# Performance work log

Measured on AMD Instinct MI355X. Metric: run time of the kernel, lower is better.

## Reference

```python
import jax, jax.numpy as jnp
import numpy as np

B = 2048
WIDTH = 128      # channel width == 1D signal length after unsqueeze
MODES = 16       # retained Fourier modes
INPUT_DIM = 100
T_DIM = 28
U_DIM = 64
NFREQ = WIDTH // 2 + 1


def setup_inputs() -> dict:
    key = jax.random.key(0)
    ks = jax.random.split(key, 32)
    rn = lambda k, s: jax.random.normal(k, s, jnp.float32)
    un = lambda k, s: jax.random.uniform(k, s, jnp.float32)
    sc_in0 = 1.0 / (1 * WIDTH)        # SpectralConv scale for conv0 (in=1)
    sc_in = 1.0 / (WIDTH * WIDTH)     # for conv1..3
    inp = {
        "X1": rn(ks[0], (B, INPUT_DIM + T_DIM)),
        "fc0_w": rn(ks[1], (WIDTH, INPUT_DIM + T_DIM)) * 0.02,
        "fc0_b": jnp.zeros((WIDTH,), jnp.float32),
        # spectral weights: torch.rand(..., cfloat) -> uniform real & imag in [0,1), scaled
        "sc0_wr": un(ks[2], (1, WIDTH, MODES)) * sc_in0,
        "sc0_wi": un(ks[3], (1, WIDTH, MODES)) * sc_in0,
        "sc1_wr": un(ks[4], (WIDTH, WIDTH, MODES)) * sc_in,
        "sc1_wi": un(ks[5], (WIDTH, WIDTH, MODES)) * sc_in,
        "sc2_wr": un(ks[6], (WIDTH, WIDTH, MODES)) * sc_in,
        "sc2_wi": un(ks[7], (WIDTH, WIDTH, MODES)) * sc_in,
        "sc3_wr": un(ks[8], (WIDTH, WIDTH, MODES)) * sc_in,
        "sc3_wi": un(ks[9], (WIDTH, WIDTH, MODES)) * sc_in,
        # pointwise (kernel-size-1) Conv1d weights as [out, in] + bias
        "w0_w": rn(ks[10], (WIDTH, 1)) * 0.02,
        "w0_b": jnp.zeros((WIDTH,), jnp.float32),
        "w1_w": rn(ks[11], (WIDTH, WIDTH)) * 0.02,
        "w1_b": jnp.zeros((WIDTH,), jnp.float32),
        "w2_w": rn(ks[12], (WIDTH, WIDTH)) * 0.02,
        "w2_b": jnp.zeros((WIDTH,), jnp.float32),
        "w3_w": rn(ks[13], (WIDTH, WIDTH)) * 0.02,
        "w3_b": jnp.zeros((WIDTH,), jnp.float32),
        "fc1_w": rn(ks[14], (WIDTH, WIDTH * WIDTH)) * 0.01,
        "fc1_b": jnp.zeros((WIDTH,), jnp.float32),
        "fc2_w": rn(ks[15], (U_DIM, WIDTH)) * 0.02,
        "fc2_b": jnp.zeros((U_DIM,), jnp.float32),
    }
    return inp


def _spectral_conv(x, wr, wi):
    # x: [B, Cin, L]; wr/wi: [Cin, Cout, MODES]
    L = x.shape[-1]
    xf = jnp.fft.rfft(x)                                   # [B, Cin, L//2+1] complex
    w = wr + 1j * wi
    of = jnp.einsum('bim,iom->bom', xf[:, :, :MODES], w)   # [B, Cout, MODES]
    of = jnp.pad(of, ((0, 0), (0, 0), (0, L // 2 + 1 - MODES)))
    return jnp.fft.irfft(of, n=L)                          # [B, Cout, L] real


def _pointwise(x, w, b):
    # kernel-size-1 Conv1d: x [B, Cin, L], w [Cout, Cin], b [Cout]
    return jnp.einsum('bil,oi->bol', x, w) + b[None, :, None]


def _gelu(x):
    return jax.nn.gelu(x, approximate=False)  # torch F.gelu default (erf)


def reference(X1, fc0_w, fc0_b, sc0_wr, sc0_wi, sc1_wr, sc1_wi, sc2_wr, sc2_wi,
              sc3_wr, sc3_wi, w0_w, w0_b, w1_w, w1_b, w2_w, w2_b, w3_w, w3_b,
              fc1_w, fc1_b, fc2_w, fc2_b):
    # fc0: lift [B, input_dim+t_dim] -> [B, width]
    x = X1 @ fc0_w.T + fc0_b
    x = x[:, None, :]  # [B, 1, WIDTH]
    x = _gelu(_spectral_conv(x, sc0_wr, sc0_wi) + _pointwise(x, w0_w, w0_b))
    x = _gelu(_spectral_conv(x, sc1_wr, sc1_wi) + _pointwise(x, w1_w, w1_b))
    x = _gelu(_spectral_conv(x, sc2_wr, sc2_wi) + _pointwise(x, w2_w, w2_b))
    x = _spectral_conv(x, sc3_wr, sc3_wi) + _pointwise(x, w3_w, w3_b)
    x = x.reshape(x.shape[0], -1)              # [B, WIDTH*WIDTH]
    x = _gelu(x @ fc1_w.T + fc1_b)
    x = x @ fc2_w.T + fc2_b                    # [B, U_DIM]
    return jnp.squeeze(x)
```

## Files before the change

### kernel.cpp

```cpp
#include <hip/hip_runtime.h>
#include <math.h>

#define PI_D 3.14159265358979323846

#define OFF_TW   0u
#define OFF_X0   4096u
#define OFF_WT   (OFF_X0 + 262144u)
#define OFF_XFR  (OFF_WT + 1572864u)
#define OFF_XFI  (OFF_XFR + 4194304u)
#define OFF_OFR  (OFF_XFI + 4194304u)
#define OFF_OFI  (OFF_OFR + 4194304u)
#define OFF_A    (OFF_OFI + 4194304u)
#define OFF_HP   OFF_XFR

__device__ __forceinline__ float gelu_f(float x) {
    return 0.5f * x * (1.0f + erff(x * 0.7071067811865476f));
}

__global__ void k_setup(float* ws) {
    int id = blockIdx.x * 256 + threadIdx.x;
    if (id < 4096) {
        int l = id >> 5, c = id & 31, m = c & 15;
        double ang = (PI_D / 64.0) * (double)((m * l) & 127);
        double v = (c < 16) ? cos(ang) : -sin(ang);
        ws[OFF_TW + id] = (float)v;
    }
}

__global__ void k_transpose(const float* w1r, const float* w1i,
                            const float* w2r, const float* w2i,
                            const float* w3r, const float* w3i, float* ws) {
    int id = blockIdx.x * 256 + threadIdx.x;
    int lay = id >> 18;
    int rem = id & 262143;
    int m = rem >> 14, i = (rem >> 7) & 127, o = rem & 127;
    const float* sr = (lay == 0) ? w1r : (lay == 1) ? w2r : w3r;
    const float* si = (lay == 0) ? w1i : (lay == 1) ? w2i : w3i;
    int src = (i * 128 + o) * 16 + m;
    ws[OFF_WT + (unsigned)lay * 524288u + rem] = sr[src];
    ws[OFF_WT + (unsigned)lay * 524288u + 262144u + rem] = si[src];
}

__global__ __launch_bounds__(256) void k_fc0(const float* X1, const float* w, const float* bias, float* ws) {
    __shared__ float xs[16][128];
    __shared__ float wsm[128][129];
    int t = threadIdx.x;
    int b0 = blockIdx.x * 16;
#pragma unroll
    for (int q = 0; q < 8; ++q) {
        int idx = q * 256 + t;
        xs[idx >> 7][idx & 127] = X1[b0 * 128 + idx];
    }
#pragma unroll
    for (int q = 0; q < 64; ++q) {
        int idx = q * 256 + t;
        wsm[idx >> 7][idx & 127] = w[idx];
    }
    __syncthreads();
    int c = t & 127, bh = t >> 7;
    float* x0 = ws + OFF_X0;
    for (int j = 0; j < 8; ++j) {
        int b = bh * 8 + j;
        float acc = bias[c];
#pragma unroll 8
        for (int k = 0; k < 128; ++k) acc += xs[b][k] * wsm[c][k];
        x0[(b0 + b) * 128 + c] = acc;
    }
}

__global__ __launch_bounds__(256) void k_layer0(const float* w0r, const float* w0i,
                                                const float* w0w, const float* w0b, float* ws) {
    __shared__ float x0s[128];
    __shared__ float tws[128][33];
    __shared__ float xrs[16], xis[16];
    __shared__ __align__(16) float ors[2048];
    __shared__ __align__(16) float ois[2048];
    int t = threadIdx.x, b = blockIdx.x;
    const float* tw = ws + OFF_TW;
    const float* x0 = ws + OFF_X0;
    if (t < 128) x0s[t] = x0[b * 128 + t];
#pragma unroll
    for (int q = 0; q < 16; ++q) {
        int idx = q * 256 + t;
        tws[idx >> 5][idx & 31] = tw[idx];
    }
    __syncthreads();
    if (t < 32) {
        float acc = 0.f;
        for (int l = 0; l < 128; ++l) acc += x0s[l] * tws[l][t];
        if (t < 16) xrs[t] = acc; else xis[t - 16] = acc;
    }
    __syncthreads();
#pragma unroll
    for (int q = 0; q < 8; ++q) {
        int idx = q * 256 + t;
        int m = idx & 15;
        float wr = w0r[idx], wi = w0i[idx];
        float sc = (m == 0) ? (1.f / 128.f) : (2.f / 128.f);
        float xr = xrs[m], xi = xis[m];
        ors[idx] = (xr * wr - xi * wi) * sc;
        ois[idx] = (xr * wi + xi * wr) * sc;
    }
    __syncthreads();
    int l = t & 127, og = t >> 7;
    float tvc[16], tvs[16];
#pragma unroll
    for (int m = 0; m < 16; ++m) { tvc[m] = tws[l][m]; tvs[m] = tws[l][16 + m]; }
    float xl = x0s[l];
    float* A = ws + OFF_A + b * 16384;
    const float4* or4 = (const float4*)ors;
    const float4* oi4 = (const float4*)ois;
    for (int oj = 0; oj < 64; ++oj) {
        int o = og * 64 + oj;
        float acc = xl * w0w[o] + w0b[o];
#pragma unroll
        for (int q = 0; q < 4; ++q) {
            float4 r4 = or4[o * 4 + q];
            float4 i4 = oi4[o * 4 + q];
            acc += r4.x * tvc[4 * q + 0] + i4.x * tvs[4 * q + 0];
            acc += r4.y * tvc[4 * q + 1] + i4.y * tvs[4 * q + 1];
            acc += r4.z * tvc[4 * q + 2] + i4.z * tvs[4 * q + 2];
            acc += r4.w * tvc[4 * q + 3] + i4.w * tvs[4 * q + 3];
        }
        A[o * 128 + l] = gelu_f(acc);
    }
}

__global__ __launch_bounds__(256) void k_dft(float* ws) {
    __shared__ float as_[16][516];
    __shared__ float tws_[16][32];
    int t = threadIdx.x;
    int row0 = blockIdx.x * 512;
    const float* A = ws + OFF_A;
    const float* tw = ws + OFF_TW;
    int tr = t >> 2, tc = t & 3;
    float acc[8][8];
#pragma unroll
    for (int j = 0; j < 8; ++j)
#pragma unroll
        for (int cc = 0; cc < 8; ++cc) acc[j][cc] = 0.f;
    for (int kc = 0; kc < 8; ++kc) {
        int k0 = kc * 16;
        __syncthreads();
#pragma unroll
        for (int q = 0; q < 8; ++q) {
            int idx = q * 256 + t;
            int r = idx >> 2, kq = idx & 3;
            float4 v = *(const float4*)&A[(row0 + r) * 128 + k0 + 4 * kq];
            as_[4 * kq + 0][r] = v.x; as_[4 * kq + 1][r] = v.y;
            as_[4 * kq + 2][r] = v.z; as_[4 * kq + 3][r] = v.w;
        }
#pragma unroll
        for (int q = 0; q < 2; ++q) {
            int idx = q * 256 + t;
            tws_[idx >> 5][idx & 31] = tw[(k0 + (idx >> 5)) * 32 + (idx & 31)];
        }
        __syncthreads();
#pragma unroll 8
        for (int kk = 0; kk < 16; ++kk) {
            float4 a0 = *(const float4*)&as_[kk][tr * 8];
            float4 a1 = *(const float4*)&as_[kk][tr * 8 + 4];
            float4 t0 = *(const float4*)&tws_[kk][tc * 8];
            float4 t1 = *(const float4*)&tws_[kk][tc * 8 + 4];
            float av[8] = {a0.x,a0.y,a0.z,a0.w,a1.x,a1.y,a1.z,a1.w};
            float tv[8] = {t0.x,t0.y,t0.z,t0.w,t1.x,t1.y,t1.z,t1.w};
#pragma unroll
            for (int j = 0; j < 8; ++j)
#pragma unroll
                for (int cc = 0; cc < 8; ++cc) acc[j][cc] += av[j] * tv[cc];
        }
    }
    float* xfr = ws + OFF_XFR;
    float* xfi = ws + OFF_XFI;
#pragma unroll
    for (int cc = 0; cc < 8; ++cc) {
        int c = tc * 8 + cc;
        float* dst = (c < 16) ? (xfr + c * 262144) : (xfi + (c - 16) * 262144);
        float4 v0 = make_float4(acc[0][cc], acc[1][cc], acc[2][cc], acc[3][cc]);
        float4 v1 = make_float4(acc[4][cc], acc[5][cc], acc[6][cc], acc[7][cc]);
        *(float4*)&dst[row0 + tr * 8] = v0;
        *(float4*)&dst[row0 + tr * 8 + 4] = v1;
    }
}

__global__ __launch_bounds__(256) void k_modemix(int lay, float* ws) {
    __shared__ float xrs[32][68], xis[32][68];
    __shared__ float wrs[32][128], wis[32][128];
    int t = threadIdx.x;
    int b0 = blockIdx.x * 64;
    int m = blockIdx.y;
    const float* xfr = ws + OFF_XFR + m * 262144;
    const float* xfi = ws + OFF_XFI + m * 262144;
    const float* wtr = ws + OFF_WT + (unsigned)lay * 524288u + m * 16384;
    const float* wti = wtr + 262144;
    int tb = t >> 4, tc = t & 15;
    float accr[4][8], acci[4][8];
#pragma unroll
    for (int jb = 0; jb < 4; ++jb)
#pragma unroll
        for (int jc = 0; jc < 8; ++jc) { accr[jb][jc] = 0.f; acci[jb][jc] = 0.f; }
    for (int kc = 0; kc < 4; ++kc) {
        int k0 = kc * 32;
        __syncthreads();
#pragma unroll
        for (int q = 0; q < 2; ++q) {
            int idx = q * 256 + t;
            int r = idx >> 3, kq = idx & 7;
            float4 vr = *(const float4*)&xfr[(b0 + r) * 128 + k0 + 4 * kq];
            float4 vi = *(const float4*)&xfi[(b0 + r) * 128 + k0 + 4 * kq];
            xrs[4*kq+0][r] = vr.x; xrs[4*kq+1][r] = vr.y; xrs[4*kq+2][r] = vr.z; xrs[4*kq+3][r] = vr.w;
            xis[4*kq+0][r] = vi.x; xis[4*kq+1][r] = vi.y; xis[4*kq+2][r] = vi.z; xis[4*kq+3][r] = vi.w;
        }
#pragma unroll
        for (int q = 0; q < 4; ++q) {
            int idx = q * 256 + t;
            int kk = idx >> 5, oq = idx & 31;
            *(float4*)&wrs[kk][4*oq] = *(const float4*)&wtr[(k0 + kk) * 128 + 4*oq];
            *(float4*)&wis[kk][4*oq] = *(const float4*)&wti[(k0 + kk) * 128 + 4*oq];
        }
        __syncthreads();
#pragma unroll 4
        for (int kk = 0; kk < 32; ++kk) {
            float4 xr4 = *(const float4*)&xrs[kk][tb * 4];
            float4 xi4 = *(const float4*)&xis[kk][tb * 4];
            float4 wr0 = *(const float4*)&wrs[kk][tc * 8];
            float4 wr1 = *(const float4*)&wrs[kk][tc * 8 + 4];
            float4 wi0 = *(const float4*)&wis[kk][tc * 8];
            float4 wi1 = *(const float4*)&wis[kk][tc * 8 + 4];
            float xrv[4] = {xr4.x, xr4.y, xr4.z, xr4.w};
            float xiv[4] = {xi4.x, xi4.y, xi4.z, xi4.w};
            float wrv[8] = {wr0.x,wr0.y,wr0.z,wr0.w,wr1.x,wr1.y,wr1.z,wr1.w};
            float wiv[8] = {wi0.x,wi0.y,wi0.z,wi0.w,wi1.x,wi1.y,wi1.z,wi1.w};
#pragma unroll
            for (int jb = 0; jb < 4; ++jb)
#pragma unroll
                for (int jc = 0; jc < 8; ++jc) {
                    accr[jb][jc] += xrv[jb] * wrv[jc] - xiv[jb] * wiv[jc];
                    acci[jb][jc] += xrv[jb] * wiv[jc] + xiv[jb] * wrv[jc];
                }
        }
    }
    float* ofr = ws + OFF_OFR + m * 262144;
    float* ofi = ws + OFF_OFI + m * 262144;
#pragma unroll
    for (int jb = 0; jb < 4; ++jb) {
        int b = b0 + tb * 4 + jb;
        float4 r0 = make_float4(accr[jb][0], accr[jb][1], accr[jb][2], accr[jb][3]);
        float4 r1 = make_float4(accr[jb][4], accr[jb][5], accr[jb][6], accr[jb][7]);
        float4 i0 = make_float4(acci[jb][0], acci[jb][1], acci[jb][2], acci[jb][3]);
        float4 i1 = make_float4(acci[jb][4], acci[jb][5], acci[jb][6], acci[jb][7]);
        *(float4*)&ofr[b * 128 + tc * 8]     = r0;
        *(float4*)&ofr[b * 128 + tc * 8 + 4] = r1;
        *(float4*)&ofi[b * 128 + tc * 8]     = i0;
        *(float4*)&ofi[b * 128 + tc * 8 + 4] = i1;
    }
}

template <int GELU>
__global__ __launch_bounds__(256) void k_layerB(const float* pw_w, const float* pw_b, float* ws) {
    __shared__ float ofr_s[16][128], ofi_s[16][128];
    __shared__ float as_[32][128];
    __shared__ float wsx[32][132];
    int t = threadIdx.x, b = blockIdx.x;
    const float* tw = ws + OFF_TW;
    float* A = ws + OFF_A + b * 16384;
    const float* ofr = ws + OFF_OFR;
    const float* ofi = ws + OFF_OFI;
    int ty = t >> 4, tx = t & 15;
    float bv[8];
#pragma unroll
    for (int jo = 0; jo < 8; ++jo) bv[jo] = pw_b[ty * 8 + jo];
#pragma unroll
    for (int q = 0; q < 2; ++q) {
        int idx = q * 256 + t;
        int mm = idx >> 5, oq = idx & 31;
        float sc = (mm == 0) ? (1.f / 128.f) : (2.f / 128.f);
        float4 vr = *(const float4*)&ofr[mm * 262144 + b * 128 + 4 * oq];
        float4 vi = *(const float4*)&ofi[mm * 262144 + b * 128 + 4 * oq];
        vr.x *= sc; vr.y *= sc; vr.z *= sc; vr.w *= sc;
        vi.x *= sc; vi.y *= sc; vi.z *= sc; vi.w *= sc;
        *(float4*)&ofr_s[mm][4 * oq] = vr;
        *(float4*)&ofi_s[mm][4 * oq] = vi;
    }
    float acc[8][8];
#pragma unroll
    for (int jo = 0; jo < 8; ++jo)
#pragma unroll
        for (int jl = 0; jl < 8; ++jl) acc[jo][jl] = 0.f;
    for (int ch = 0; ch < 4; ++ch) {
        int i0 = ch * 32;
        __syncthreads();
#pragma unroll
        for (int q = 0; q < 4; ++q) {
            int idx = q * 256 + t;
            int ic = idx >> 5, lq = idx & 31;
            *(float4*)&as_[ic][4 * lq] = *(const float4*)&A[(i0 + ic) * 128 + 4 * lq];
        }
#pragma unroll
        for (int q = 0; q < 4; ++q) {
            int idx = q * 256 + t;
            int o = idx >> 3, iq = idx & 7;
            float4 v = *(const float4*)&pw_w[o * 128 + i0 + 4 * iq];
            wsx[4*iq+0][o] = v.x; wsx[4*iq+1][o] = v.y; wsx[4*iq+2][o] = v.z; wsx[4*iq+3][o] = v.w;
        }
        __syncthreads();
#pragma unroll 4
        for (int ic = 0; ic < 32; ++ic) {
            float4 a0 = *(const float4*)&as_[ic][tx * 8];
            float4 a1 = *(const float4*)&as_[ic][tx * 8 + 4];
            float4 w0 = *(const float4*)&wsx[ic][ty * 8];
            float4 w1 = *(const float4*)&wsx[ic][ty * 8 + 4];
            float av[8] = {a0.x,a0.y,a0.z,a0.w,a1.x,a1.y,a1.z,a1.w};
            float wv[8] = {w0.x,w0.y,w0.z,w0.w,w1.x,w1.y,w1.z,w1.w};
#pragma unroll
            for (int jo = 0; jo < 8; ++jo)
#pragma unroll
                for (int jl = 0; jl < 8; ++jl) acc[jo][jl] += wv[jo] * av[jl];
        }
    }
    __syncthreads();
    float (*twsA)[33] = (float(*)[33])wsx;
#pragma unroll
    for (int q = 0; q < 4; ++q) {
        int idx = q * 256 + t;
        int l = idx >> 3, cq = idx & 7;
        float4 v = *(const float4*)&tw[l * 32 + 4 * cq];
        twsA[l][4*cq+0] = v.x; twsA[l][4*cq+1] = v.y; twsA[l][4*cq+2] = v.z; twsA[l][4*cq+3] = v.w;
    }
    __syncthreads();
#pragma unroll 2
    for (int m = 0; m < 16; ++m) {
        float orv[8], oiv[8];
#pragma unroll
        for (int jo = 0; jo < 8; ++jo) { orv[jo] = ofr_s[m][ty * 8 + jo]; oiv[jo] = ofi_s[m][ty * 8 + jo]; }
        float cv[8], sv[8];
#pragma unroll
        for (int jl = 0; jl < 8; ++jl) {
            int l = tx * 8 + jl;
            cv[jl] = twsA[l][m]; sv[jl] = twsA[l][16 + m];
        }
#pragma unroll
        for (int jo = 0; jo < 8; ++jo)
#pragma unroll
            for (int jl = 0; jl < 8; ++jl) acc[jo][jl] += orv[jo] * cv[jl] + oiv[jo] * sv[jl];
    }
#pragma unroll
    for (int jo = 0; jo < 8; ++jo) {
        int o = ty * 8 + jo;
        float v[8];
#pragma unroll
        for (int jl = 0; jl < 8; ++jl) {
            float x = acc[jo][jl] + bv[jo];
            v[jl] = GELU ? gelu_f(x) : x;
        }
        *(float4*)&A[o * 128 + tx * 8]     = make_float4(v[0], v[1], v[2], v[3]);
        *(float4*)&A[o * 128 + tx * 8 + 4] = make_float4(v[4], v[5], v[6], v[7]);
    }
}

__global__ __launch_bounds__(256) void k_fc12(const float* fc1w, float* ws) {
    __shared__ float as_[32][132];
    __shared__ float ws_[32][132];
    int t = threadIdx.x;
    int b0 = blockIdx.x * 128;
    int kz = blockIdx.y;
    const float* A = ws + OFF_A;
    int tm = t >> 4, tn = t & 15;
    float acc[8][8];
#pragma unroll
    for (int jb = 0; jb < 8; ++jb)
#pragma unroll
        for (int jc = 0; jc < 8; ++jc) acc[jb][jc] = 0.f;
    for (int ks = 0; ks < 8; ++ks) {
        int k0 = kz * 256 + ks * 32;
        __syncthreads();
#pragma unroll
        for (int q = 0; q < 4; ++q) {
            int idx = q * 256 + t;
            int r = idx >> 3, kq = idx & 7;
            float4 v = *(const float4*)&A[(b0 + r) * 16384 + k0 + 4 * kq];
            as_[4*kq+0][r] = v.x; as_[4*kq+1][r] = v.y; as_[4*kq+2][r] = v.z; as_[4*kq+3][r] = v.w;
        }
#pragma unroll
        for (int q = 0; q < 4; ++q) {
            int idx = q * 256 + t;
            int c = idx >> 3, kq = idx & 7;
            float4 v = *(const float4*)&fc1w[c * 16384 + k0 + 4 * kq];
            ws_[4*kq+0][c] = v.x; ws_[4*kq+1][c] = v.y; ws_[4*kq+2][c] = v.z; ws_[4*kq+3][c] = v.w;
        }
        __syncthreads();
#pragma unroll 4
        for (int kk = 0; kk < 32; ++kk) {
            float4 a0 = *(const float4*)&as_[kk][tm * 8];
            float4 a1 = *(const float4*)&as_[kk][tm * 8 + 4];
            float4 w0 = *(const float4*)&ws_[kk][tn * 8];
            float4 w1 = *(const float4*)&ws_[kk][tn * 8 + 4];
            float av[8] = {a0.x,a0.y,a0.z,a0.w,a1.x,a1.y,a1.z,a1.w};
            float wv[8] = {w0.x,w0.y,w0.z,w0.w,w1.x,w1.y,w1.z,w1.w};
#pragma unroll
            for (int jb = 0; jb < 8; ++jb)
#pragma unroll
                for (int jc = 0; jc < 8; ++jc) acc[jb][jc] += av[jb] * wv[jc];
        }
    }
    float* hp = ws + OFF_HP + kz * 262144;
#pragma unroll
    for (int jb = 0; jb < 8; ++jb) {
        int b = b0 + tm * 8 + jb;
        *(float4*)&hp[b * 128 + tn * 8]     = make_float4(acc[jb][0], acc[jb][1], acc[jb][2], acc[jb][3]);
        *(float4*)&hp[b * 128 + tn * 8 + 4] = make_float4(acc[jb][4], acc[jb][5], acc[jb][6], acc[jb][7]);
    }
}

__global__ __launch_bounds__(256) void k_fc2(const float* fc1b, const float* fc2w, const float* fc2b,
                                             float* ws, float* out) {
    __shared__ float hs[8][128];
    __shared__ float w2s[64][129];
    int t = threadIdx.x;
    int b0 = blockIdx.x * 8;
    const float* hp = ws + OFF_HP;
#pragma unroll
    for (int q = 0; q < 4; ++q) {
        int idx = q * 256 + t;
        int bb = idx >> 7, c = idx & 127;
        float s = fc1b[c];
#pragma unroll 8
        for (int kz = 0; kz < 64; ++kz) s += hp[kz * 262144 + (b0 + bb) * 128 + c];
        hs[bb][c] = gelu_f(s);
    }
#pragma unroll
    for (int q = 0; q < 32; ++q) {
        int idx = q * 256 + t;
        w2s[idx >> 7][idx & 127] = fc2w[idx];
    }
    __syncthreads();
#pragma unroll
    for (int q = 0; q < 2; ++q) {
        int idx = q * 256 + t;
        int bb = idx >> 6, u = idx & 63;
        float acc = fc2b[u];
#pragma unroll 8
        for (int c = 0; c < 128; ++c) acc += hs[bb][c] * w2s[u][c];
        out[(b0 + bb) * 64 + u] = acc;
    }
}

extern "C" void kernel_launch(void* const* d_in, const int* in_sizes, int n_in,
                              void* d_out, int out_size, void* d_ws, size_t ws_size,
                              hipStream_t stream) {
    const float* X1   = (const float*)d_in[0];
    const float* fc0w = (const float*)d_in[1];
    const float* fc0b = (const float*)d_in[2];
    const float* s0r  = (const float*)d_in[3];
    const float* s0i  = (const float*)d_in[4];
    const float* s1r  = (const float*)d_in[5];
    const float* s1i  = (const float*)d_in[6];
    const float* s2r  = (const float*)d_in[7];
    const float* s2i  = (const float*)d_in[8];
    const float* s3r  = (const float*)d_in[9];
    const float* s3i  = (const float*)d_in[10];
    const float* w0w  = (const float*)d_in[11];
    const float* w0b  = (const float*)d_in[12];
    const float* w1w  = (const float*)d_in[13];
    const float* w1b  = (const float*)d_in[14];
    const float* w2w  = (const float*)d_in[15];
    const float* w2b  = (const float*)d_in[16];
    const float* w3w  = (const float*)d_in[17];
    const float* w3b  = (const float*)d_in[18];
    const float* fc1w = (const float*)d_in[19];
    const float* fc1b = (const float*)d_in[20];
    const float* fc2w = (const float*)d_in[21];
    const float* fc2b = (const float*)d_in[22];
    float* ws  = (float*)d_ws;
    float* out = (float*)d_out;

    k_setup<<<dim3(16), dim3(256), 0, stream>>>(ws);
    k_transpose<<<dim3(3072), dim3(256), 0, stream>>>(s1r, s1i, s2r, s2i, s3r, s3i, ws);
    k_fc0<<<dim3(128), dim3(256), 0, stream>>>(X1, fc0w, fc0b, ws);
    k_layer0<<<dim3(2048), dim3(256), 0, stream>>>(s0r, s0i, w0w, w0b, ws);

    const float* pww[3] = {w1w, w2w, w3w};
    const float* pwb[3] = {w1b, w2b, w3b};
    for (int lay = 0; lay < 3; ++lay) {
        k_dft<<<dim3(512), dim3(256), 0, stream>>>(ws);
        k_modemix<<<dim3(32, 16), dim3(256), 0, stream>>>(lay, ws);
        if (lay < 2)
            k_layerB<1><<<dim3(2048), dim3(256), 0, stream>>>(pww[lay], pwb[lay], ws);
        else
            k_layerB<0><<<dim3(2048), dim3(256), 0, stream>>>(pww[lay], pwb[lay], ws);
    }

    k_fc12<<<dim3(16, 64), dim3(256), 0, stream>>>(fc1w, ws);
    k_fc2<<<dim3(256), dim3(256), 0, stream>>>(fc1b, fc2w, fc2b, ws, out);
}
```

Before: 1.094 ms.

## Swizzle shared-memory tiles, pre-transpose pointwise weights and twiddles, shrink DFT blocks

Adds an XOR swizzle on float4 columns for the shared tiles in the DFT, mode-mix, layerB and fc1 kernels, meant to remove LDS bank conflicts on the vectorised reads. A new prep kernel pre-transposes the pointwise conv weights and the twiddle table so layerB can load them with coalesced float4 copies. layerB now computes the inverse DFT first from a transposed twiddle tile and shares one buffer with the later GEMM. The DFT kernel moves to 128-thread blocks over 256 rows, and the first barrier in each k-loop is dropped. The cost is an extra kernel launch and more index arithmetic.

```diff
diff --git a/kernel.cpp b/kernel.cpp
--- a/kernel.cpp
+++ b/kernel.cpp
@@ -5,6 +5,8 @@
 
 #define OFF_TW   0u
 #define OFF_X0   4096u
+#define OFF_PWT  OFF_X0
+#define OFF_TWT  (OFF_X0 + 49152u)
 #define OFF_WT   (OFF_X0 + 262144u)
 #define OFF_XFR  (OFF_WT + 1572864u)
 #define OFF_XFI  (OFF_XFR + 4194304u)
@@ -16,6 +18,8 @@
 __device__ __forceinline__ float gelu_f(float x) {
     return 0.5f * x * (1.0f + erff(x * 0.7071067811865476f));
 }
+
+__device__ __forceinline__ int swzc(int c4) { return 4 * (c4 ^ ((c4 >> 3) & 3)); }
 
 __global__ void k_setup(float* ws) {
     int id = blockIdx.x * 256 + threadIdx.x;
@@ -41,6 +45,20 @@
     ws[OFF_WT + (unsigned)lay * 524288u + 262144u + rem] = si[src];
 }
 
+__global__ void k_prep2(const float* w1w, const float* w2w, const float* w3w, float* ws) {
+    int id = blockIdx.x * 256 + threadIdx.x;
+    if (id < 49152) {
+        int lay = id >> 14, rem = id & 16383;
+        int i = rem >> 7, o = rem & 127;
+        const float* w = (lay == 0) ? w1w : (lay == 1) ? w2w : w3w;
+        ws[OFF_PWT + id] = w[o * 128 + i];
+    } else if (id < 53248) {
+        int id2 = id - 49152;
+        int c = id2 >> 7, l = id2 & 127;
+        ws[OFF_TWT + c * 128 + l] = ws[OFF_TW + l * 32 + c];
+    }
+}
+
 __global__ __launch_bounds__(256) void k_fc0(const float* X1, const float* w, const float* bias, float* ws) {
     __shared__ float xs[16][128];
     __shared__ float wsm[128][129];
@@ -126,11 +144,11 @@
     }
 }
 
-__global__ __launch_bounds__(256) void k_dft(float* ws) {
-    __shared__ float as_[16][516];
+__global__ __launch_bounds__(128) void k_dft(float* ws) {
+    __shared__ float as_[16][260];
     __shared__ float tws_[16][32];
     int t = threadIdx.x;
-    int row0 = blockIdx.x * 512;
+    int row0 = blockIdx.x * 256;
     const float* A = ws + OFF_A;
     const float* tw = ws + OFF_TW;
     int tr = t >> 2, tc = t & 3;
@@ -139,27 +157,29 @@
     for (int j = 0; j < 8; ++j)
 #pragma unroll
         for (int cc = 0; cc < 8; ++cc) acc[j][cc] = 0.f;
+    int col0 = swzc(2 * tr), col1 = swzc(2 * tr + 1);
     for (int kc = 0; kc < 8; ++kc) {
         int k0 = kc * 16;
-        __syncthreads();
+        if (kc) __syncthreads();
 #pragma unroll
         for (int q = 0; q < 8; ++q) {
-            int idx = q * 256 + t;
+            int idx = q * 128 + t;
             int r = idx >> 2, kq = idx & 3;
             float4 v = *(const float4*)&A[(row0 + r) * 128 + k0 + 4 * kq];
-            as_[4 * kq + 0][r] = v.x; as_[4 * kq + 1][r] = v.y;
-            as_[4 * kq + 2][r] = v.z; as_[4 * kq + 3][r] = v.w;
-        }
-#pragma unroll
-        for (int q = 0; q < 2; ++q) {
-            int idx = q * 256 + t;
+            int sc = swzc(r >> 2) + (r & 3);
+            as_[4 * kq + 0][sc] = v.x; as_[4 * kq + 1][sc] = v.y;
+            as_[4 * kq + 2][sc] = v.z; as_[4 * kq + 3][sc] = v.w;
+        }
+#pragma unroll
+        for (int q = 0; q < 4; ++q) {
+            int idx = q * 128 + t;
             tws_[idx >> 5][idx & 31] = tw[(k0 + (idx >> 5)) * 32 + (idx & 31)];
         }
         __syncthreads();
 #pragma unroll 8
         for (int kk = 0; kk < 16; ++kk) {
-            float4 a0 = *(const float4*)&as_[kk][tr * 8];
-            float4 a1 = *(const float4*)&as_[kk][tr * 8 + 4];
+            float4 a0 = *(const float4*)&as_[kk][col0];
+            float4 a1 = *(const float4*)&as_[kk][col1];
             float4 t0 = *(const float4*)&tws_[kk][tc * 8];
             float4 t1 = *(const float4*)&tws_[kk][tc * 8 + 4];
             float av[8] = {a0.x,a0.y,a0.z,a0.w,a1.x,a1.y,a1.z,a1.w};
@@ -185,7 +205,7 @@
 
 __global__ __launch_bounds__(256) void k_modemix(int lay, float* ws) {
     __shared__ float xrs[32][68], xis[32][68];
-    __shared__ float wrs[32][128], wis[32][128];
+    __shared__ float wrs[32][132], wis[32][132];
     int t = threadIdx.x;
     int b0 = blockIdx.x * 64;
     int m = blockIdx.y;
@@ -194,6 +214,7 @@
     const float* wtr = ws + OFF_WT + (unsigned)lay * 524288u + m * 16384;
     const float* wti = wtr + 262144;
     int tb = t >> 4, tc = t & 15;
+    int wc0 = swzc(2 * tc), wc1 = swzc(2 * tc + 1);
     float accr[4][8], acci[4][8];
 #pragma unroll
     for (int jb = 0; jb < 4; ++jb)
@@ -201,7 +222,7 @@
         for (int jc = 0; jc < 8; ++jc) { accr[jb][jc] = 0.f; acci[jb][jc] = 0.f; }
     for (int kc = 0; kc < 4; ++kc) {
         int k0 = kc * 32;
-        __syncthreads();
+        if (kc) __syncthreads();
 #pragma unroll
         for (int q = 0; q < 2; ++q) {
             int idx = q * 256 + t;
@@ -215,18 +236,18 @@
         for (int q = 0; q < 4; ++q) {
             int idx = q * 256 + t;
             int kk = idx >> 5, oq = idx & 31;
-            *(float4*)&wrs[kk][4*oq] = *(const float4*)&wtr[(k0 + kk) * 128 + 4*oq];
-            *(float4*)&wis[kk][4*oq] = *(const float4*)&wti[(k0 + kk) * 128 + 4*oq];
+            *(float4*)&wrs[kk][swzc(oq)] = *(const float4*)&wtr[(k0 + kk) * 128 + 4 * oq];
+            *(float4*)&wis[kk][swzc(oq)] = *(const float4*)&wti[(k0 + kk) * 128 + 4 * oq];
         }
         __syncthreads();
 #pragma unroll 4
         for (int kk = 0; kk < 32; ++kk) {
             float4 xr4 = *(const float4*)&xrs[kk][tb * 4];
             float4 xi4 = *(const float4*)&xis[kk][tb * 4];
-            float4 wr0 = *(const float4*)&wrs[kk][tc * 8];
-            float4 wr1 = *(const float4*)&wrs[kk][tc * 8 + 4];
-            float4 wi0 = *(const float4*)&wis[kk][tc * 8];
-            float4 wi1 = *(const float4*)&wis[kk][tc * 8 + 4];
+            float4 wr0 = *(const float4*)&wrs[kk][wc0];
+            float4 wr1 = *(const float4*)&wrs[kk][wc1];
+            float4 wi0 = *(const float4*)&wis[kk][wc0];
+            float4 wi1 = *(const float4*)&wis[kk][wc1];
             float xrv[4] = {xr4.x, xr4.y, xr4.z, xr4.w};
             float xiv[4] = {xi4.x, xi4.y, xi4.z, xi4.w};
             float wrv[8] = {wr0.x,wr0.y,wr0.z,wr0.w,wr1.x,wr1.y,wr1.z,wr1.w};
@@ -257,19 +278,18 @@
 }
 
 template <int GELU>
-__global__ __launch_bounds__(256) void k_layerB(const float* pw_w, const float* pw_b, float* ws) {
-    __shared__ float ofr_s[16][128], ofi_s[16][128];
-    __shared__ float as_[32][128];
-    __shared__ float wsx[32][132];
+__global__ __launch_bounds__(256) void k_layerB(const float* pwt, const float* pw_b, float* ws) {
+    __shared__ float smem[8448];
     int t = threadIdx.x, b = blockIdx.x;
-    const float* tw = ws + OFF_TW;
-    float* A = ws + OFF_A + b * 16384;
+    float* A = ws + OFF_A + (unsigned)b * 16384u;
     const float* ofr = ws + OFF_OFR;
     const float* ofi = ws + OFF_OFI;
+    const float* twt = ws + OFF_TWT;
     int ty = t >> 4, tx = t & 15;
-    float bv[8];
-#pragma unroll
-    for (int jo = 0; jo < 8; ++jo) bv[jo] = pw_b[ty * 8 + jo];
+    int col0 = swzc(2 * tx), col1 = swzc(2 * tx + 1);
+    float* ofr_s = smem;
+    float* ofi_s = smem + 2048;
+    float* twTs  = smem + 4096;
 #pragma unroll
     for (int q = 0; q < 2; ++q) {
         int idx = q * 256 + t;
@@ -279,37 +299,65 @@
         float4 vi = *(const float4*)&ofi[mm * 262144 + b * 128 + 4 * oq];
         vr.x *= sc; vr.y *= sc; vr.z *= sc; vr.w *= sc;
         vi.x *= sc; vi.y *= sc; vi.z *= sc; vi.w *= sc;
-        *(float4*)&ofr_s[mm][4 * oq] = vr;
-        *(float4*)&ofi_s[mm][4 * oq] = vi;
-    }
+        *(float4*)&ofr_s[mm * 128 + 4 * oq] = vr;
+        *(float4*)&ofi_s[mm * 128 + 4 * oq] = vi;
+    }
+#pragma unroll
+    for (int q = 0; q < 4; ++q) {
+        int idx = q * 256 + t;
+        int row = idx >> 5, c4 = idx & 31;
+        *(float4*)&twTs[row * 132 + swzc(c4)] = *(const float4*)&twt[row * 128 + 4 * c4];
+    }
+    __syncthreads();
     float acc[8][8];
 #pragma unroll
     for (int jo = 0; jo < 8; ++jo)
 #pragma unroll
         for (int jl = 0; jl < 8; ++jl) acc[jo][jl] = 0.f;
+#pragma unroll 2
+    for (int m = 0; m < 16; ++m) {
+        float4 or0 = *(const float4*)&ofr_s[m * 128 + ty * 8];
+        float4 or1 = *(const float4*)&ofr_s[m * 128 + ty * 8 + 4];
+        float4 oi0 = *(const float4*)&ofi_s[m * 128 + ty * 8];
+        float4 oi1 = *(const float4*)&ofi_s[m * 128 + ty * 8 + 4];
+        float4 c0 = *(const float4*)&twTs[m * 132 + col0];
+        float4 c1 = *(const float4*)&twTs[m * 132 + col1];
+        float4 s0 = *(const float4*)&twTs[(16 + m) * 132 + col0];
+        float4 s1 = *(const float4*)&twTs[(16 + m) * 132 + col1];
+        float orv[8] = {or0.x,or0.y,or0.z,or0.w,or1.x,or1.y,or1.z,or1.w};
+        float oiv[8] = {oi0.x,oi0.y,oi0.z,oi0.w,oi1.x,oi1.y,oi1.z,oi1.w};
+        float cv[8]  = {c0.x,c0.y,c0.z,c0.w,c1.x,c1.y,c1.z,c1.w};
+        float sv[8]  = {s0.x,s0.y,s0.z,s0.w,s1.x,s1.y,s1.z,s1.w};
+#pragma unroll
+        for (int jo = 0; jo < 8; ++jo)
+#pragma unroll
+            for (int jl = 0; jl < 8; ++jl) acc[jo][jl] += orv[jo] * cv[jl] + oiv[jo] * sv[jl];
+    }
+    __syncthreads();
+    float* as_ = smem;
+    float* wsx = smem + 4224;
     for (int ch = 0; ch < 4; ++ch) {
         int i0 = ch * 32;
-        __syncthreads();
+        if (ch) __syncthreads();
 #pragma unroll
         for (int q = 0; q < 4; ++q) {
             int idx = q * 256 + t;
             int ic = idx >> 5, lq = idx & 31;
-            *(float4*)&as_[ic][4 * lq] = *(const float4*)&A[(i0 + ic) * 128 + 4 * lq];
+            *(float4*)&as_[ic * 132 + swzc(lq)] = *(const float4*)&A[(i0 + ic) * 128 + 4 * lq];
         }
 #pragma unroll
         for (int q = 0; q < 4; ++q) {
             int idx = q * 256 + t;
-            int o = idx >> 3, iq = idx & 7;
-            float4 v = *(const float4*)&pw_w[o * 128 + i0 + 4 * iq];
-            wsx[4*iq+0][o] = v.x; wsx[4*iq+1][o] = v.y; wsx[4*iq+2][o] = v.z; wsx[4*iq+3][o] = v.w;
+            int ic = idx >> 5, oq = idx & 31;
+            *(float4*)&wsx[ic * 132 + 4 * oq] = *(const float4*)&pwt[(i0 + ic) * 128 + 4 * oq];
         }
         __syncthreads();
 #pragma unroll 4
         for (int ic = 0; ic < 32; ++ic) {
-            float4 a0 = *(const float4*)&as_[ic][tx * 8];
-            float4 a1 = *(const float4*)&as_[ic][tx * 8 + 4];
-            float4 w0 = *(const float4*)&wsx[ic][ty * 8];
-            float4 w1 = *(const float4*)&wsx[ic][ty * 8 + 4];
+            float4 a0 = *(const float4*)&as_[ic * 132 + col0];
+            float4 a1 = *(const float4*)&as_[ic * 132 + col1];
+            float4 w0 = *(const float4*)&wsx[ic * 132 + ty * 8];
+            float4 w1 = *(const float4*)&wsx[ic * 132 + ty * 8 + 4];
             float av[8] = {a0.x,a0.y,a0.z,a0.w,a1.x,a1.y,a1.z,a1.w};
             float wv[8] = {w0.x,w0.y,w0.z,w0.w,w1.x,w1.y,w1.z,w1.w};
 #pragma unroll
@@ -318,39 +366,14 @@
                 for (int jl = 0; jl < 8; ++jl) acc[jo][jl] += wv[jo] * av[jl];
         }
     }
-    __syncthreads();
-    float (*twsA)[33] = (float(*)[33])wsx;
-#pragma unroll
-    for (int q = 0; q < 4; ++q) {
-        int idx = q * 256 + t;
-        int l = idx >> 3, cq = idx & 7;
-        float4 v = *(const float4*)&tw[l * 32 + 4 * cq];
-        twsA[l][4*cq+0] = v.x; twsA[l][4*cq+1] = v.y; twsA[l][4*cq+2] = v.z; twsA[l][4*cq+3] = v.w;
-    }
-    __syncthreads();
-#pragma unroll 2
-    for (int m = 0; m < 16; ++m) {
-        float orv[8], oiv[8];
-#pragma unroll
-        for (int jo = 0; jo < 8; ++jo) { orv[jo] = ofr_s[m][ty * 8 + jo]; oiv[jo] = ofi_s[m][ty * 8 + jo]; }
-        float cv[8], sv[8];
-#pragma unroll
-        for (int jl = 0; jl < 8; ++jl) {
-            int l = tx * 8 + jl;
-            cv[jl] = twsA[l][m]; sv[jl] = twsA[l][16 + m];
-        }
-#pragma unroll
-        for (int jo = 0; jo < 8; ++jo)
-#pragma unroll
-            for (int jl = 0; jl < 8; ++jl) acc[jo][jl] += orv[jo] * cv[jl] + oiv[jo] * sv[jl];
-    }
 #pragma unroll
     for (int jo = 0; jo < 8; ++jo) {
         int o = ty * 8 + jo;
+        float bv = pw_b[o];
         float v[8];
 #pragma unroll
         for (int jl = 0; jl < 8; ++jl) {
-            float x = acc[jo][jl] + bv[jo];
+            float x = acc[jo][jl] + bv;
             v[jl] = GELU ? gelu_f(x) : x;
         }
         *(float4*)&A[o * 128 + tx * 8]     = make_float4(v[0], v[1], v[2], v[3]);
@@ -366,6 +389,7 @@
     int kz = blockIdx.y;
     const float* A = ws + OFF_A;
     int tm = t >> 4, tn = t & 15;
+    int wc0 = swzc(2 * tn), wc1 = swzc(2 * tn + 1);
     float acc[8][8];
 #pragma unroll
     for (int jb = 0; jb < 8; ++jb)
@@ -373,7 +397,7 @@
         for (int jc = 0; jc < 8; ++jc) acc[jb][jc] = 0.f;
     for (int ks = 0; ks < 8; ++ks) {
         int k0 = kz * 256 + ks * 32;
-        __syncthreads();
+        if (ks) __syncthreads();
 #pragma unroll
         for (int q = 0; q < 4; ++q) {
             int idx = q * 256 + t;
@@ -386,15 +410,16 @@
             int idx = q * 256 + t;
             int c = idx >> 3, kq = idx & 7;
             float4 v = *(const float4*)&fc1w[c * 16384 + k0 + 4 * kq];
-            ws_[4*kq+0][c] = v.x; ws_[4*kq+1][c] = v.y; ws_[4*kq+2][c] = v.z; ws_[4*kq+3][c] = v.w;
+            int sc = swzc(c >> 2) + (c & 3);
+            ws_[4*kq+0][sc] = v.x; ws_[4*kq+1][sc] = v.y; ws_[4*kq+2][sc] = v.z; ws_[4*kq+3][sc] = v.w;
         }
         __syncthreads();
 #pragma unroll 4
         for (int kk = 0; kk < 32; ++kk) {
             float4 a0 = *(const float4*)&as_[kk][tm * 8];
             float4 a1 = *(const float4*)&as_[kk][tm * 8 + 4];
-            float4 w0 = *(const float4*)&ws_[kk][tn * 8];
-            float4 w1 = *(const float4*)&ws_[kk][tn * 8 + 4];
+            float4 w0 = *(const float4*)&ws_[kk][wc0];
+            float4 w1 = *(const float4*)&ws_[kk][wc1];
             float av[8] = {a0.x,a0.y,a0.z,a0.w,a1.x,a1.y,a1.z,a1.w};
             float wv[8] = {w0.x,w0.y,w0.z,w0.w,w1.x,w1.y,w1.z,w1.w};
 #pragma unroll
@@ -478,16 +503,17 @@
     k_transpose<<<dim3(3072), dim3(256), 0, stream>>>(s1r, s1i, s2r, s2i, s3r, s3i, ws);
     k_fc0<<<dim3(128), dim3(256), 0, stream>>>(X1, fc0w, fc0b, ws);
     k_layer0<<<dim3(2048), dim3(256), 0, stream>>>(s0r, s0i, w0w, w0b, ws);
-
-    const float* pww[3] = {w1w, w2w, w3w};
+    k_prep2<<<dim3(208), dim3(256), 0, stream>>>(w1w, w2w, w3w, ws);
+
     const float* pwb[3] = {w1b, w2b, w3b};
     for (int lay = 0; lay < 3; ++lay) {
-        k_dft<<<dim3(512), dim3(256), 0, stream>>>(ws);
+        k_dft<<<dim3(1024), dim3(128), 0, stream>>>(ws);
         k_modemix<<<dim3(32, 16), dim3(256), 0, stream>>>(lay, ws);
+        const float* pwt = ws + OFF_PWT + (unsigned)lay * 16384u;
         if (lay < 2)
-            k_layerB<1><<<dim3(2048), dim3(256), 0, stream>>>(pww[lay], pwb[lay], ws);
+            k_layerB<1><<<dim3(2048), dim3(256), 0, stream>>>(pwt, pwb[lay], ws);
         else
-            k_layerB<0><<<dim3(2048), dim3(256), 0, stream>>>(pww[lay], pwb[lay], ws);
+            k_layerB<0><<<dim3(2048), dim3(256), 0, stream>>>(pwt, pwb[lay], ws);
     }
 
     k_fc12<<<dim3(16, 64), dim3(256), 0, stream>>>(fc1w, ws);
```

New measurement: 1.100 ms. Within noise of the previous version (+0.5%).
